# Kernel optimization log

Hardware: AMD Instinct MI355X
Metric: run time of the kernel (lower is better)

Reference implementation:

```python
import jax, jax.numpy as jnp
import numpy as np

B, F, D = 16384, 32, 64   # batch, n_continuous_features, input_dim
H = 2 * D                  # hidden = 2*input_dim per the d_hidden spec


def setup_inputs() -> dict:
    key = jax.random.key(0)
    ks = jax.random.split(key, 6)
    s1 = 1.0 / np.sqrt(D).astype(np.float32)
    s2 = 1.0 / np.sqrt(H).astype(np.float32)
    return {
        "X": jax.random.normal(ks[0], (B, F), jnp.float32),
        "r_": jax.random.normal(ks[1], (B, F, D), jnp.float32),
        # stacked per-feature weights (one tiny MLP per continuous column)
        "W1": jax.random.normal(ks[2], (F, D, H), jnp.float32) * s1,
        "b1": jax.random.normal(ks[3], (F, H), jnp.float32) * s1,
        "W2": jax.random.normal(ks[4], (F, H, 1), jnp.float32) * s2,
        "b2": jax.random.normal(ks[5], (F, 1), jnp.float32) * s2,
    }


def reference(X, r_, W1, b1, W2, b2):
    # Per-feature 2-layer MLP (Linear->relu->Linear->relu), batched over the
    # feature axis instead of the original Python loop over ModuleDict.
    h = jax.nn.relu(jnp.einsum('bfd,fdh->bfh', r_, W1) + b1)   # [B,F,H]
    y = jax.nn.relu(jnp.einsum('bfh,fho->bfo', h, W2) + b2)    # [B,F,1]
    x = X[..., None]                                           # [B,F,1] raw scalar per column
    # Original returns list of (x_col, mlp_out) pairs; we pack them as [B,F,2]
    # with [...,0]=x and [...,1]=mlp output (same values, dense layout).
    return jnp.concatenate([x, y], axis=-1)
```

## Files before the change

### kernel.cpp

```cpp
#include <hip/hip_runtime.h>
#include <stdint.h>

#define B_SZ 16384
#define F_SZ 32
#define D_SZ 64
#define H_SZ 128
#define RSTRIDE 72

typedef __attribute__((ext_vector_type(8))) short  short8;
typedef __attribute__((ext_vector_type(4))) float  float4v;
typedef __attribute__((ext_vector_type(4))) unsigned int uint4v;

__device__ __forceinline__ unsigned int pkbf(float lo, float hi) {
  unsigned int ulo = __builtin_bit_cast(unsigned int, lo) + 0x8000u;
  unsigned int uhi = __builtin_bit_cast(unsigned int, hi) + 0x8000u;
  return __builtin_amdgcn_perm(uhi, ulo, 0x07060302u);
}

__global__ __launch_bounds__(256) void ContMlp_prep(
    const float* __restrict__ W1, const float* __restrict__ b1,
    const float* __restrict__ W2, unsigned short* __restrict__ w1t,
    unsigned int* __restrict__ bw) {
  const int f  = blockIdx.x >> 2;
  const int hq = blockIdx.x & 3;
  const int h0 = hq * 32;
  const int t  = threadIdx.x;
  __shared__ float lds[D_SZ][33];
  const float* w1f = W1 + (size_t)f * (D_SZ * H_SZ);
#pragma unroll
  for (int i = 0; i < 8; ++i) {
    int idx = t + 256 * i;
    int d = idx >> 5, hh = idx & 31;
    lds[d][hh] = w1f[d * H_SZ + h0 + hh];
  }
  __syncthreads();
  unsigned short* o = w1t + (size_t)f * (H_SZ * D_SZ);
#pragma unroll
  for (int i = 0; i < 8; ++i) {
    int idx = t + 256 * i;
    int hh = idx >> 6, d = idx & 63;
    unsigned int u = __builtin_bit_cast(unsigned int, lds[d][hh]) + 0x8000u;
    o[(h0 + hh) * D_SZ + d] = (unsigned short)(u >> 16);
  }
  if (hq == 0 && t < H_SZ) {
    unsigned int ub = __builtin_bit_cast(unsigned int, b1[f * H_SZ + t]) + 0x8000u;
    unsigned int uw = __builtin_bit_cast(unsigned int, W2[f * H_SZ + t]) + 0x8000u;
    bw[f * H_SZ + t] = (ub & 0xFFFF0000u) | (uw >> 16);
  }
}

__global__ __launch_bounds__(256) void ContMlp_main(
    const float* __restrict__ r_,
    const unsigned short* __restrict__ w1t, const unsigned int* __restrict__ bw,
    const float* __restrict__ b2, float* __restrict__ ydst,
    int y_fmul, int y_rmul, int y_cadd) {
  const int f    = blockIdx.x & 31;
  const int tile = blockIdx.x >> 5;
  const int w    = threadIdx.x >> 6;
  const int l    = threadIdx.x & 63;
  const int col  = l & 15;
  const int quad = l >> 4;

  __shared__ unsigned short w1l[H_SZ * RSTRIDE];
  __shared__ unsigned int   bwl[H_SZ];
  __shared__ float          rbuf[4][1024];

  {
    const uint4v* src = (const uint4v*)(w1t + (size_t)f * (H_SZ * D_SZ));
#pragma unroll
    for (int i = 0; i < 4; ++i) {
      int ci = threadIdx.x + 256 * i;
      int h = ci >> 3, dc = ci & 7;
      *(uint4v*)(w1l + h * RSTRIDE + dc * 8) = src[ci];
    }
    if (threadIdx.x < H_SZ) bwl[threadIdx.x] = bw[f * H_SZ + threadIdx.x];
  }
  __syncthreads();
  const float b2f = b2[f];

  const int row_w0 = tile * 512 + w * 128;
  const float* gl = r_ + (size_t)(row_w0 + col) * (F_SZ * D_SZ)
                       + f * D_SZ + quad * 4;
  float* rb = &rbuf[w][0];
  float yv[8];

#pragma unroll 1
  for (int s = 0; s < 8; ++s) {
    const float* gs = gl + (size_t)s * 16 * (F_SZ * D_SZ);
#pragma unroll
    for (int i = 0; i < 4; ++i) {
      __builtin_amdgcn_global_load_lds(
          (const __attribute__((address_space(1))) void*)(gs + i * 16),
          (__attribute__((address_space(3))) void*)(rb + i * 256),
          16, 0, 0);
    }
    __builtin_amdgcn_s_waitcnt(0x0F70);

    float4v f0 = *(const float4v*)(rb + (quad * 2) * 64 + col * 4);
    float4v f1 = *(const float4v*)(rb + (quad * 2 + 1) * 64 + col * 4);
    float4v f2 = *(const float4v*)(rb + (8 + quad * 2) * 64 + col * 4);
    float4v f3 = *(const float4v*)(rb + (9 + quad * 2) * 64 + col * 4);
    uint4v bq0 = {pkbf(f0.x, f0.y), pkbf(f0.z, f0.w),
                  pkbf(f1.x, f1.y), pkbf(f1.z, f1.w)};
    uint4v bq1 = {pkbf(f2.x, f2.y), pkbf(f2.z, f2.w),
                  pkbf(f3.x, f3.y), pkbf(f3.z, f3.w)};
    short8 bf0 = __builtin_bit_cast(short8, bq0);
    short8 bf1 = __builtin_bit_cast(short8, bq1);

    float ysum = 0.f;
#pragma unroll
    for (int t = 0; t < 8; ++t) {
      const unsigned short* wrow = w1l + (col + 16 * t) * RSTRIDE + quad * 8;
      short8 a0 = *(const short8*)(wrow);
      short8 a1 = *(const short8*)(wrow + 32);
      float4v acc = {0.f, 0.f, 0.f, 0.f};
      acc = __builtin_amdgcn_mfma_f32_16x16x32_bf16(a0, bf0, acc, 0, 0, 0);
      acc = __builtin_amdgcn_mfma_f32_16x16x32_bf16(a1, bf1, acc, 0, 0, 0);
      uint4v bwv = *(const uint4v*)(bwl + 16 * t + quad * 4);
#pragma unroll
      for (int r = 0; r < 4; ++r) {
        unsigned int u = bwv[r];
        float b1v = __builtin_bit_cast(float, u & 0xFFFF0000u);
        float w2v = __builtin_bit_cast(float, u << 16);
        ysum = fmaf(fmaxf(acc[r] + b1v, 0.f), w2v, ysum);
      }
    }
    ysum += __shfl_xor(ysum, 16, 64);
    ysum += __shfl_xor(ysum, 32, 64);
    yv[s] = fmaxf(ysum + b2f, 0.f);
  }

  if (quad == 0) {
#pragma unroll
    for (int s = 0; s < 8; ++s) {
      float* yp = ydst + (size_t)f * y_fmul
                       + (size_t)(row_w0 + s * 16 + col) * y_rmul + y_cadd;
      *yp = yv[s];
    }
  }
}

__global__ __launch_bounds__(256) void ContMlp_combine(
    const float* __restrict__ X, const float* __restrict__ yws,
    float* __restrict__ out) {
  __shared__ float yl[F_SZ][33];
  const int r0 = blockIdx.x * 32;
  const int t = threadIdx.x;
#pragma unroll
  for (int i = 0; i < 4; ++i) {
    int idx = t + 256 * i;
    int f = idx >> 5, r = idx & 31;
    yl[f][r] = yws[(size_t)f * B_SZ + r0 + r];
  }
  __syncthreads();
#pragma unroll
  for (int i = 0; i < 4; ++i) {
    int idx = t + 256 * i;
    int r = idx >> 5, f = idx & 31;
    float2 o2 = make_float2(X[(size_t)(r0 + r) * F_SZ + f], yl[f][r]);
    *(float2*)(out + (size_t)(r0 + r) * (2 * F_SZ) + 2 * f) = o2;
  }
}

__global__ __launch_bounds__(256) void ContMlp_xwrite(
    const float* __restrict__ X, float* __restrict__ out) {
  int idx = blockIdx.x * 256 + threadIdx.x;
  int r = idx >> 5, f = idx & 31;
  out[(size_t)r * (2 * F_SZ) + 2 * f] = X[idx];
}

extern "C" void kernel_launch(void* const* d_in, const int* in_sizes, int n_in,
                              void* d_out, int out_size, void* d_ws, size_t ws_size,
                              hipStream_t stream) {
  const float* X  = (const float*)d_in[0];
  const float* r_ = (const float*)d_in[1];
  const float* W1 = (const float*)d_in[2];
  const float* b1 = (const float*)d_in[3];
  const float* W2 = (const float*)d_in[4];
  const float* b2 = (const float*)d_in[5];
  float* out = (float*)d_out;

  const size_t w1t_bytes = (size_t)F_SZ * H_SZ * D_SZ * 2;
  const size_t bw_off    = w1t_bytes;
  const size_t bw_bytes  = (size_t)F_SZ * H_SZ * 4;
  const size_t y_off     = bw_off + bw_bytes;
  const size_t y_bytes   = (size_t)B_SZ * F_SZ * 4;

  unsigned short* w1t = (unsigned short*)d_ws;
  unsigned int*   bw  = (unsigned int*)((char*)d_ws + bw_off);

  ContMlp_prep<<<F_SZ * 4, 256, 0, stream>>>(W1, b1, W2, w1t, bw);

  if (ws_size >= y_off + y_bytes) {
    float* yws = (float*)((char*)d_ws + y_off);
    ContMlp_main<<<32 * F_SZ, 256, 0, stream>>>(r_, w1t, bw, b2, yws,
                                                B_SZ, 1, 0);
    ContMlp_combine<<<B_SZ / 32, 256, 0, stream>>>(X, yws, out);
  } else {
    ContMlp_main<<<32 * F_SZ, 256, 0, stream>>>(r_, w1t, bw, b2, out,
                                                2, 2 * F_SZ, 1);
    ContMlp_xwrite<<<(B_SZ * F_SZ) / 256, 256, 0, stream>>>(X, out);
  }
}
```

Baseline: 213.7 us.

## Double-buffer r_ loads, hold W1 fragments in registers, shrink blocks

The main kernel now double-buffers the global-to-LDS loads of r_, so the next 16-row slab is in flight while the current one runs through MFMA. The W1 A-fragments and packed bias/W2 values are loaded once into registers instead of being re-read from LDS every iteration. Blocks shrink to 128 threads (2 waves) with twice as many blocks, and y is stored per iteration. The extra register-resident fragments raise VGPR pressure, which may lower occupancy, and each block reloads W1 for fewer rows.

After: 217.0 us. No clear change (+1.5%).

```diff
diff --git a/kernel.cpp b/kernel.cpp
--- a/kernel.cpp
+++ b/kernel.cpp
@@ -5,7 +5,6 @@
 #define F_SZ 32
 #define D_SZ 64
 #define H_SZ 128
-#define RSTRIDE 72
 
 typedef __attribute__((ext_vector_type(8))) short  short8;
 typedef __attribute__((ext_vector_type(4))) float  float4v;
@@ -49,7 +48,7 @@
   }
 }
 
-__global__ __launch_bounds__(256) void ContMlp_main(
+__global__ __launch_bounds__(128) void ContMlp_main(
     const float* __restrict__ r_,
     const unsigned short* __restrict__ w1t, const unsigned int* __restrict__ bw,
     const float* __restrict__ b2, float* __restrict__ ydst,
@@ -61,40 +60,59 @@
   const int col  = l & 15;
   const int quad = l >> 4;
 
-  __shared__ unsigned short w1l[H_SZ * RSTRIDE];
+  __shared__ unsigned short w1l[H_SZ * D_SZ];
   __shared__ unsigned int   bwl[H_SZ];
-  __shared__ float          rbuf[4][1024];
+  __shared__ float          rbuf[2][2][1024];
 
   {
     const uint4v* src = (const uint4v*)(w1t + (size_t)f * (H_SZ * D_SZ));
-#pragma unroll
-    for (int i = 0; i < 4; ++i) {
-      int ci = threadIdx.x + 256 * i;
-      int h = ci >> 3, dc = ci & 7;
-      *(uint4v*)(w1l + h * RSTRIDE + dc * 8) = src[ci];
-    }
-    if (threadIdx.x < H_SZ) bwl[threadIdx.x] = bw[f * H_SZ + threadIdx.x];
+    uint4v* dst = (uint4v*)w1l;
+#pragma unroll
+    for (int i = 0; i < 8; ++i)
+      dst[threadIdx.x + 128 * i] = src[threadIdx.x + 128 * i];
+    bwl[threadIdx.x] = bw[f * H_SZ + threadIdx.x];
   }
   __syncthreads();
+
+  short8 afrag[8][2];
+#pragma unroll
+  for (int t = 0; t < 8; ++t)
+#pragma unroll
+    for (int ks = 0; ks < 2; ++ks)
+      afrag[t][ks] = *(const short8*)(w1l + (col + 16 * t) * D_SZ + ks * 32 + quad * 8);
+  uint4v bwreg[8];
+#pragma unroll
+  for (int t = 0; t < 8; ++t)
+    bwreg[t] = *(const uint4v*)(bwl + 16 * t + quad * 4);
   const float b2f = b2[f];
 
-  const int row_w0 = tile * 512 + w * 128;
+  const int row_w0 = tile * 256 + w * 128;
   const float* gl = r_ + (size_t)(row_w0 + col) * (F_SZ * D_SZ)
                        + f * D_SZ + quad * 4;
-  float* rb = &rbuf[w][0];
-  float yv[8];
+
+#define ISSUE(S, HALF)                                                       \
+  do {                                                                       \
+    const float* gs_ = gl + (size_t)(S) * 16 * (F_SZ * D_SZ);                \
+    float* rb_ = &rbuf[w][HALF][0];                                          \
+    _Pragma("unroll")                                                        \
+    for (int i_ = 0; i_ < 4; ++i_)                                           \
+      __builtin_amdgcn_global_load_lds(                                      \
+          (const __attribute__((address_space(1))) void*)(gs_ + i_ * 16),    \
+          (__attribute__((address_space(3))) void*)(rb_ + i_ * 256),         \
+          16, 0, 0);                                                         \
+  } while (0)
+
+  ISSUE(0, 0);
 
 #pragma unroll 1
   for (int s = 0; s < 8; ++s) {
-    const float* gs = gl + (size_t)s * 16 * (F_SZ * D_SZ);
-#pragma unroll
-    for (int i = 0; i < 4; ++i) {
-      __builtin_amdgcn_global_load_lds(
-          (const __attribute__((address_space(1))) void*)(gs + i * 16),
-          (__attribute__((address_space(3))) void*)(rb + i * 256),
-          16, 0, 0);
+    if (s < 7) {
+      ISSUE(s + 1, (s + 1) & 1);
+      __builtin_amdgcn_s_waitcnt(0x0F74);
+    } else {
+      __builtin_amdgcn_s_waitcnt(0x0F70);
     }
-    __builtin_amdgcn_s_waitcnt(0x0F70);
+    const float* rb = &rbuf[w][s & 1][0];
 
     float4v f0 = *(const float4v*)(rb + (quad * 2) * 64 + col * 4);
     float4v f1 = *(const float4v*)(rb + (quad * 2 + 1) * 64 + col * 4);
@@ -110,16 +128,12 @@
     float ysum = 0.f;
 #pragma unroll
     for (int t = 0; t < 8; ++t) {
-      const unsigned short* wrow = w1l + (col + 16 * t) * RSTRIDE + quad * 8;
-      short8 a0 = *(const short8*)(wrow);
-      short8 a1 = *(const short8*)(wrow + 32);
       float4v acc = {0.f, 0.f, 0.f, 0.f};
-      acc = __builtin_amdgcn_mfma_f32_16x16x32_bf16(a0, bf0, acc, 0, 0, 0);
-      acc = __builtin_amdgcn_mfma_f32_16x16x32_bf16(a1, bf1, acc, 0, 0, 0);
-      uint4v bwv = *(const uint4v*)(bwl + 16 * t + quad * 4);
+      acc = __builtin_amdgcn_mfma_f32_16x16x32_bf16(afrag[t][0], bf0, acc, 0, 0, 0);
+      acc = __builtin_amdgcn_mfma_f32_16x16x32_bf16(afrag[t][1], bf1, acc, 0, 0, 0);
 #pragma unroll
       for (int r = 0; r < 4; ++r) {
-        unsigned int u = bwv[r];
+        unsigned int u = bwreg[t][r];
         float b1v = __builtin_bit_cast(float, u & 0xFFFF0000u);
         float w2v = __builtin_bit_cast(float, u << 16);
         ysum = fmaf(fmaxf(acc[r] + b1v, 0.f), w2v, ysum);
@@ -127,17 +141,14 @@
     }
     ysum += __shfl_xor(ysum, 16, 64);
     ysum += __shfl_xor(ysum, 32, 64);
-    yv[s] = fmaxf(ysum + b2f, 0.f);
-  }
-
-  if (quad == 0) {
-#pragma unroll
-    for (int s = 0; s < 8; ++s) {
+    float y = fmaxf(ysum + b2f, 0.f);
+    if (quad == 0) {
       float* yp = ydst + (size_t)f * y_fmul
                        + (size_t)(row_w0 + s * 16 + col) * y_rmul + y_cadd;
-      *yp = yv[s];
+      *yp = y;
     }
   }
+#undef ISSUE
 }
 
 __global__ __launch_bounds__(256) void ContMlp_combine(
@@ -193,11 +204,11 @@
 
   if (ws_size >= y_off + y_bytes) {
     float* yws = (float*)((char*)d_ws + y_off);
-    ContMlp_main<<<32 * F_SZ, 256, 0, stream>>>(r_, w1t, bw, b2, yws,
+    ContMlp_main<<<64 * F_SZ, 128, 0, stream>>>(r_, w1t, bw, b2, yws,
                                                 B_SZ, 1, 0);
     ContMlp_combine<<<B_SZ / 32, 256, 0, stream>>>(X, yws, out);
   } else {
-    ContMlp_main<<<32 * F_SZ, 256, 0, stream>>>(r_, w1t, bw, b2, out,
+    ContMlp_main<<<64 * F_SZ, 128, 0, stream>>>(r_, w1t, bw, b2, out,
                                                 2, 2 * F_SZ, 1);
     ContMlp_xwrite<<<(B_SZ * F_SZ) / 256, 256, 0, stream>>>(X, out);
   }
```
